# Kernel optimization log

Hardware: AMD Instinct MI355X
Metric: run time of the kernel (lower is better)

Reference implementation:

```python
import jax, jax.numpy as jnp
import numpy as np

NC = 2            # num_classes
CONF_THR = 0.7
IOU_THR = 0.2

_PI, _PJ = np.triu_indices(9, k=1)   # 36 candidate edge directions for min-area rect


def _decode_level(out, stride):
    # out: [C,h,w]; scale (x,y) channels by stride and add the pixel grid, flatten to [h*w, C]
    C, h, w = out.shape
    gw = (stride * jnp.arange(w, dtype=out.dtype))[None, :]
    gh = (stride * jnp.arange(h, dtype=out.dtype))[:, None]
    out = out.at[NC + 1].set(out[NC + 1] * stride + gw)
    out = out.at[NC + 2].set(out[NC + 2] * stride + gh)
    return out.reshape(C, -1).T


def _min_area_polygons(pts18):
    # pts18: (N,18) interleaved (a,b) coordinate pairs of 9 points.
    # Min-area enclosing rectangle: optimal rect is aligned with some point-pair direction;
    # brute-force all 36 pairs (superset of hull edges) -> exact result, fully vectorized.
    P = pts18.reshape(-1, 9, 2)                       # (N,9,2)
    d = P[:, _PJ] - P[:, _PI]                         # (N,36,2)
    nrm = jnp.sqrt(jnp.sum(d * d, -1) + 1e-12)
    c, s = d[..., 0] / nrm, d[..., 1] / nrm           # (N,36)
    a, b = P[..., 0][:, None, :], P[..., 1][:, None, :]   # (N,1,9)
    u = a * c[..., None] + b * s[..., None]           # rotate by -theta
    v = -a * s[..., None] + b * c[..., None]
    umin, umax = u.min(-1), u.max(-1)
    vmin, vmax = v.min(-1), v.max(-1)
    area = (umax - umin) * (vmax - vmin)              # (N,36)
    k = jnp.argmin(area, 1)[:, None]
    tk = lambda z: jnp.take_along_axis(z, k, 1)[:, 0]
    c, s, umin, umax, vmin, vmax = map(tk, (c, s, umin, umax, vmin, vmax))
    cu = jnp.stack([umin, umax, umax, umin], -1)      # rect corners in rotated frame
    cv = jnp.stack([vmin, vmin, vmax, vmax], -1)
    ca = cu * c[:, None] - cv * s[:, None]            # rotate back
    cb = cu * s[:, None] + cv * c[:, None]
    return jnp.stack([ca, cb], -1).reshape(-1, 8)     # (N,8) interleaved corners


def _points_in_quad(pts, quad):
    # pts (M,2), quad (4,2) convex with consistent winding -> (M,) bool
    e = jnp.roll(quad, -1, 0) - quad
    r = pts[:, None, :] - quad[None]
    cr = e[None, :, 0] * r[..., 1] - e[None, :, 1] * r[..., 0]
    return (cr >= 0).all(-1) | (cr <= 0).all(-1)


def _box_decoder(rect):
    # rect (N,8) -> (N,5) [cx, cy, w, h, angle]; y_first=True convention from the source
    w = jnp.sqrt((rect[:, 0] - rect[:, 2]) ** 2 + (rect[:, 1] - rect[:, 3]) ** 2)
    h = jnp.sqrt((rect[:, 4] - rect[:, 2]) ** 2 + (rect[:, 5] - rect[:, 3]) ** 2)
    cx = rect[:, 1:8:2].sum(1) * 0.25
    cy = rect[:, 0:8:2].sum(1) * 0.25
    ang = jnp.arctan((rect[:, 0] - rect[:, 2]) / (rect[:, 1] - rect[:, 3]))
    return jnp.stack([cx, cy, w, h, ang], -1)


def _rbox_corners(b):
    cx, cy, w, h, a = b[0], b[1], b[2], b[3], b[4]
    cs, sn = jnp.cos(a), jnp.sin(a)
    lx = jnp.array([-0.5, 0.5, 0.5, -0.5]) * w
    ly = jnp.array([-0.5, -0.5, 0.5, 0.5]) * h
    return jnp.stack([cx + lx * cs - ly * sn, cy + lx * sn + ly * cs], -1)  # (4,2)


def _quad_inter_area(A, B):
    # exact intersection area of two convex quads A,B (4,2):
    # candidates = corners of each inside the other + all 16 edge-edge intersections,
    # sorted by angle around their centroid, masked shoelace.
    inA = _points_in_quad(B, A)
    inB = _points_in_quad(A, B)
    rA = jnp.roll(A, -1, 0) - A
    rB = jnp.roll(B, -1, 0) - B
    qp = B[None] - A[:, None]                                  # (4,4,2)
    den = rA[:, None, 0] * rB[None, :, 1] - rA[:, None, 1] * rB[None, :, 0]
    dsafe = jnp.where(jnp.abs(den) < 1e-9, 1e-9, den)
    t = (qp[..., 0] * rB[None, :, 1] - qp[..., 1] * rB[None, :, 0]) / dsafe
    uu = (qp[..., 0] * rA[:, None, 1] - qp[..., 1] * rA[:, None, 0]) / dsafe
    okx = (jnp.abs(den) > 1e-9) & (t >= 0) & (t <= 1) & (uu >= 0) & (uu <= 1)
    X = A[:, None] + t[..., None] * rA[:, None]
    pts = jnp.concatenate([A, B, X.reshape(16, 2)], 0)          # (24,2)
    val = jnp.concatenate([inB, inA, okx.reshape(16)], 0)
    n = val.sum()
    cen = jnp.sum(jnp.where(val[:, None], pts, 0.0), 0) / jnp.maximum(n, 1)
    rel = pts - cen
    ang = jnp.where(val, jnp.arctan2(rel[:, 1], rel[:, 0]), 1e9)
    o = jnp.argsort(ang)
    rp, vs = rel[o], val[o]
    rp = jnp.where(vs[:, None], rp, rp[0])   # invalid slots -> first valid vertex (zero-area edges)
    nx = jnp.roll(rp, -1, 0)
    area = 0.5 * jnp.abs(jnp.sum(rp[:, 0] * nx[:, 1] - rp[:, 1] * nx[:, 0]))
    return jnp.where(n >= 3, area, 0.0)


def _forward(out3, out4, out5, off1_l3, off1_l4, off1_l5, offf_l3, offf_l4, offf_l5):
    outs = jnp.concatenate([_decode_level(out3[0], 4),
                            _decode_level(out4[0], 8),
                            _decode_level(out5[0], 16)], 0)          # (N, NC+3)
    flat = lambda z: z[0].reshape(18, -1).T
    off1 = jnp.concatenate([flat(off1_l3), flat(off1_l4), flat(off1_l5)], 0)
    offf = jnp.concatenate([flat(offf_l3), flat(offf_l4), flat(offf_l5)], 0) + off1
    N = outs.shape[0]
    x, y = outs[:, NC + 1], outs[:, NC + 2]
    offf = offf + jnp.tile(jnp.stack([y, x], -1), (1, 9))            # (y,x) interleaved, 9 points
    xs, ys = offf[:, 1:18:2], offf[:, 0:18:2]
    area = (xs.max(1) - xs.min(1)) * (ys.max(1) - ys.min(1)) / 40.0
    conf = outs[:, 0]
    conf_mask = conf > CONF_THR * jax.nn.sigmoid(area)
    rect = _min_area_polygons(offf)                                  # (N,8)
    boxes5 = _box_decoder(rect)                                      # (N,5)
    corners = jax.vmap(_rbox_corners)(boxes5)                        # (N,4,2)
    areas5 = boxes5[:, 2] * boxes5[:, 3]
    position = outs[:, NC + 1:]                                      # (N,2) = (x,y)
    pts_yx = jnp.stack([position[:, 1], position[:, 0]], -1)         # (y,x), matches rect plane
    quads = rect.reshape(N, 4, 2)
    order = jnp.argsort(jnp.where(conf_mask, conf, -jnp.inf))[::-1]

    def step(carry, i):
        suppressed, keep = carry
        active = jnp.logical_not(suppressed[i])
        keep = keep.at[i].set(active)
        inside = _points_in_quad(pts_yx, quads[i])                   # points_in_polygons
        inter = jax.vmap(lambda C: _quad_inter_area(corners[i], C))(corners)
        iou = inter / (areas5[i] + areas5 - inter + 1e-9)            # box_iou_rotated
        suppressed = suppressed | (active & (inside | (iou >= IOU_THR)))
        return (suppressed, keep), None

    init = (jnp.logical_not(conf_mask), jnp.zeros(N, dtype=bool))
    (_, keep), _ = jax.lax.scan(step, init, order)

    cls = outs[:, 1:NC + 1]
    maxc = cls.max(1)
    masks = jnp.stack([keep & (cls[:, i] == maxc) for i in range(NC)], 0)  # (NC,N)
    cnt = masks.sum(1)
    result = jnp.where(masks[:, :, None], position[None], 0.0)             # (NC,N,2) padded
    rect_out = rect * keep[:, None].astype(rect.dtype)                     # (N,8) padded
    return cnt, result, rect_out


def setup_inputs() -> dict:
    key = jax.random.key(0)
    shapes = [("out3", (1, NC + 3, 32, 32)), ("out4", (1, NC + 3, 16, 16)), ("out5", (1, NC + 3, 8, 8)),
              ("off1_l3", (1, 18, 32, 32)), ("off1_l4", (1, 18, 16, 16)), ("off1_l5", (1, 18, 8, 8)),
              ("offf_l3", (1, 18, 32, 32)), ("offf_l4", (1, 18, 16, 16)), ("offf_l5", (1, 18, 8, 8))]
    ks = jax.random.split(key, len(shapes))
    return {n: jax.random.normal(k, s, dtype=jnp.float32) for (n, s), k in zip(shapes, ks)}


def reference(out3, out4, out5, off1_l3, off1_l4, off1_l5, offf_l3, offf_l4, offf_l5):
    return _forward(out3, out4, out5, off1_l3, off1_l4, off1_l5, offf_l3, offf_l4, offf_l5)
```

## Files before the change

### kernel.cpp

```cpp
#include <hip/hip_runtime.h>
#include <math.h>

#define N_DET 1344
#define NW 21
#define MW_MAX 8
#define T2S 9
#define PAIR_CAP 40000


__device__ __forceinline__ bool pt_in_quad4(const float* qx, const float* qy,
                                            float px, float py) {
    bool allp = true, alln = true;
#pragma unroll
    for (int k = 0; k < 4; k++) {
        int k1 = (k + 1) & 3;
        float ex = qx[k1] - qx[k], ey = qy[k1] - qy[k];
        float rx = px - qx[k],     ry = py - qy[k];
        float cr = ex * ry - ey * rx;
        allp = allp && (cr >= 0.f);
        alln = alln && (cr <= 0.f);
    }
    return allp || alln;
}

__device__ float quad_inter_area(const float* Ax, const float* Ay,
                                 const float* Bx, const float* By) {
    float px[24], py[24];
    unsigned vmask = 0;
    int n = 0;
#pragma unroll
    for (int k = 0; k < 4; k++) {
        px[k] = Ax[k]; py[k] = Ay[k];
        if (pt_in_quad4(Bx, By, Ax[k], Ay[k])) { vmask |= 1u << k; n++; }
    }
#pragma unroll
    for (int k = 0; k < 4; k++) {
        px[4 + k] = Bx[k]; py[4 + k] = By[k];
        if (pt_in_quad4(Ax, Ay, Bx[k], By[k])) { vmask |= 1u << (4 + k); n++; }
    }
#pragma unroll
    for (int k = 0; k < 4; k++) {
        int k1 = (k + 1) & 3;
        float rax = Ax[k1] - Ax[k], ray = Ay[k1] - Ay[k];
#pragma unroll
        for (int l = 0; l < 4; l++) {
            int l1 = (l + 1) & 3;
            float rbx = Bx[l1] - Bx[l], rby = By[l1] - By[l];
            float qpx = Bx[l] - Ax[k],  qpy = By[l] - Ay[k];
            float den = rax * rby - ray * rbx;
            float ad  = fabsf(den);
            float dsafe = (ad < 1e-9f) ? 1e-9f : den;
            float t = (qpx * rby - qpy * rbx) / dsafe;
            float u = (qpx * ray - qpy * rax) / dsafe;
            bool ok = (ad > 1e-9f) && t >= 0.f && t <= 1.f && u >= 0.f && u <= 1.f;
            int id = 8 + k * 4 + l;
            px[id] = Ax[k] + t * rax;
            py[id] = Ay[k] + t * ray;
            if (ok) { vmask |= 1u << id; n++; }
        }
    }
    float cx = 0.f, cy = 0.f;
#pragma unroll
    for (int m = 0; m < 24; m++)
        if ((vmask >> m) & 1u) { cx += px[m]; cy += py[m]; }
    int mx = (n < 1) ? 1 : n;
    cx = cx / (float)mx;
    cy = cy / (float)mx;

    unsigned long long key[32];
    float sx[32], sy[32];
#pragma unroll
    for (int m = 0; m < 24; m++) {
        float rx = px[m] - cx, ry = py[m] - cy;
        float a = ((vmask >> m) & 1u) ? atan2f(ry, rx) : 1e9f;
        unsigned u = __float_as_uint(a);
        u = (u & 0x80000000u) ? ~u : (u | 0x80000000u);
        key[m] = (((unsigned long long)u) << 6) | (unsigned)m;
        sx[m] = rx; sy[m] = ry;
    }
#pragma unroll
    for (int m = 24; m < 32; m++) { key[m] = ~0ull; sx[m] = 0.f; sy[m] = 0.f; }

#pragma unroll
    for (int k = 2; k <= 32; k <<= 1) {
#pragma unroll
        for (int j = k >> 1; j > 0; j >>= 1) {
#pragma unroll
            for (int t = 0; t < 32; t++) {
                int l = t ^ j;
                if (l > t) {
                    bool up = ((t & k) == 0);
                    bool sw = up ? (key[t] > key[l]) : (key[t] < key[l]);
                    if (sw) {
                        unsigned long long tk = key[t]; key[t] = key[l]; key[l] = tk;
                        float tx = sx[t]; sx[t] = sx[l]; sx[l] = tx;
                        float ty = sy[t]; sy[t] = sy[l]; sy[l] = ty;
                    }
                }
            }
        }
    }

    unsigned ut = __float_as_uint(1e9f) | 0x80000000u;
    unsigned long long kt = ((unsigned long long)ut) << 6;
    float fx = sx[0], fy = sy[0];
    float qx2[24], qy2[24];
#pragma unroll
    for (int m = 0; m < 24; m++) {
        bool v = key[m] < kt;
        qx2[m] = v ? sx[m] : fx;
        qy2[m] = v ? sy[m] : fy;
    }
    float ssum = 0.f;
#pragma unroll
    for (int m = 0; m < 24; m++) {
        int m1 = (m + 1) % 24;
        ssum += qx2[m] * qy2[m1] - qy2[m] * qx2[m1];
    }
    float area = 0.5f * fabsf(ssum);
    return (n >= 3) ? area : 0.f;
}

__device__ bool iou_suppress(const float* __restrict__ cor, const float* __restrict__ a5,
                             int i, int j) {
    float Axr[4], Ayr[4], Bxr[4], Byr[4];
#pragma unroll
    for (int k = 0; k < 4; k++) {
        Axr[k] = cor[i * 8 + 2 * k]; Ayr[k] = cor[i * 8 + 2 * k + 1];
        Bxr[k] = cor[j * 8 + 2 * k]; Byr[k] = cor[j * 8 + 2 * k + 1];
    }
    float inter = quad_inter_area(Axr, Ayr, Bxr, Byr);
    float iou = inter / (a5[i] + a5[j] - inter + 1e-9f);
    return iou >= 0.2f;
}

__global__ void k_decode(const float* __restrict__ out3, const float* __restrict__ out4,
                         const float* __restrict__ out5,
                         const float* __restrict__ o1l3, const float* __restrict__ o1l4,
                         const float* __restrict__ o1l5,
                         const float* __restrict__ ofl3, const float* __restrict__ ofl4,
                         const float* __restrict__ ofl5,
                         float* conf, float* cls0, float* cls1, float* xx, float* yy,
                         float* a5, float* ccx, float* ccy, float* rr,
                         float* rect, float* cor, int* mask, int* Mcnt, int* pairCnt) {
    int n = blockIdx.x * blockDim.x + threadIdx.x;
    if (n >= N_DET) return;
    if (n == 0) { *Mcnt = 0; *pairCnt = 0; }
    const float *out, *o1, *of;
    int w, idx; float stride;
    if (n < 1024)      { out = out3; o1 = o1l3; of = ofl3; w = 32; idx = n;        stride = 4.f; }
    else if (n < 1280) { out = out4; o1 = o1l4; of = ofl4; w = 16; idx = n - 1024; stride = 8.f; }
    else               { out = out5; o1 = o1l5; of = ofl5; w = 8;  idx = n - 1280; stride = 16.f; }
    int hw = w * w;
    int row = idx / w, col = idx % w;
    float cf = out[0 * hw + idx];
    float c0 = out[1 * hw + idx];
    float c1 = out[2 * hw + idx];
    float x  = out[3 * hw + idx] * stride + stride * (float)col;
    float y  = out[4 * hw + idx] * stride + stride * (float)row;

    float Pa[9], Pb[9];
    float minb = INFINITY, maxb = -INFINITY, mina = INFINITY, maxa = -INFINITY;
#pragma unroll
    for (int k = 0; k < 9; k++) {
        float a = of[(2 * k) * hw + idx]     + o1[(2 * k) * hw + idx]     + y;
        float b = of[(2 * k + 1) * hw + idx] + o1[(2 * k + 1) * hw + idx] + x;
        Pa[k] = a; Pb[k] = b;
        mina = fminf(mina, a); maxa = fmaxf(maxa, a);
        minb = fminf(minb, b); maxb = fmaxf(maxb, b);
    }
    float area = (maxb - minb) * (maxa - mina) / 40.0f;
    float sg = 1.0f / (1.0f + expf(-area));
    int m = (cf > 0.7f * sg) ? 1 : 0;

    float best = INFINITY, bc = 0.f, bs = 0.f;
    float bumin = 0.f, bumax = 0.f, bvmin = 0.f, bvmax = 0.f;
#pragma unroll
    for (int i = 0; i < 9; i++) {
#pragma unroll
        for (int j = i + 1; j < 9; j++) {
            float d0 = Pa[j] - Pa[i], d1 = Pb[j] - Pb[i];
            float nr = sqrtf(d0 * d0 + d1 * d1 + 1e-12f);
            float c = d0 / nr, s = d1 / nr;
            float umin = INFINITY, umax = -INFINITY, vmin = INFINITY, vmax = -INFINITY;
#pragma unroll
            for (int k = 0; k < 9; k++) {
                float u =  Pa[k] * c + Pb[k] * s;
                float v = -Pa[k] * s + Pb[k] * c;
                umin = fminf(umin, u); umax = fmaxf(umax, u);
                vmin = fminf(vmin, v); vmax = fmaxf(vmax, v);
            }
            float ar = (umax - umin) * (vmax - vmin);
            if (ar < best) { best = ar; bc = c; bs = s;
                             bumin = umin; bumax = umax; bvmin = vmin; bvmax = vmax; }
        }
    }
    float cu[4] = {bumin, bumax, bumax, bumin};
    float cv[4] = {bvmin, bvmin, bvmax, bvmax};
    float r8[8];
#pragma unroll
    for (int k = 0; k < 4; k++) {
        r8[2 * k]     = cu[k] * bc - cv[k] * bs;
        r8[2 * k + 1] = cu[k] * bs + cv[k] * bc;
    }
    float w5 = sqrtf((r8[0] - r8[2]) * (r8[0] - r8[2]) + (r8[1] - r8[3]) * (r8[1] - r8[3]));
    float h5 = sqrtf((r8[4] - r8[2]) * (r8[4] - r8[2]) + (r8[5] - r8[3]) * (r8[5] - r8[3]));
    float cx = (r8[1] + r8[3] + r8[5] + r8[7]) * 0.25f;
    float cy = (r8[0] + r8[2] + r8[4] + r8[6]) * 0.25f;
    float ang = atanf((r8[0] - r8[2]) / (r8[1] - r8[3]));
    float cs = cosf(ang), sn = sinf(ang);
    const float lxs[4] = {-0.5f, 0.5f, 0.5f, -0.5f};
    const float lys[4] = {-0.5f, -0.5f, 0.5f, 0.5f};
#pragma unroll
    for (int k = 0; k < 4; k++) {
        cor[n * 8 + 2 * k]     = cx + lxs[k] * w5 * cs - lys[k] * h5 * sn;
        cor[n * 8 + 2 * k + 1] = cy + lxs[k] * w5 * sn + lys[k] * h5 * cs;
    }
#pragma unroll
    for (int k = 0; k < 8; k++) rect[n * 8 + k] = r8[k];
    conf[n] = cf; cls0[n] = c0; cls1[n] = c1;
    xx[n] = x; yy[n] = y; a5[n] = w5 * h5; mask[n] = m;
    ccx[n] = cx; ccy[n] = cy;
    rr[n] = 0.5f * sqrtf(w5 * w5 + h5 * h5);
}

__global__ __launch_bounds__(64) void k_order(const float* __restrict__ conf,
                                              const int* __restrict__ mask,
                                              int* order, int* Mcnt) {
    int b = blockIdx.x;
    int lane = threadIdx.x;
    int mb = mask[b];
    float ki = mb ? conf[b] : -INFINITY;
    int rank = 0;
    for (int j = lane; j < N_DET; j += 64) {
        float kj = mask[j] ? conf[j] : -INFINITY;
        rank += ((kj > ki) || (kj == ki && j > b)) ? 1 : 0;
    }
    for (int off = 32; off; off >>= 1) rank += __shfl_down(rank, off, 64);
    if (lane == 0) {
        order[rank] = b;
        if (mb) atomicAdd(Mcnt, 1);
    }
}

__global__ __launch_bounds__(256) void k_pairs_a(
        const float* __restrict__ rect, const float* __restrict__ cor,
        const float* __restrict__ a5,
        const float* __restrict__ xx, const float* __restrict__ yy,
        const float* __restrict__ ccx, const float* __restrict__ ccy,
        const float* __restrict__ rr,
        const int* __restrict__ order, const int* __restrict__ Mcnt,
        unsigned long long* __restrict__ S2, unsigned int* __restrict__ pairs,
        int* __restrict__ pairCnt) {
    int gw   = (blockIdx.x * 256 + threadIdx.x) >> 6;
    int lane = threadIdx.x & 63;
    int M = *Mcnt;
    int MW = (M + 63) >> 6;
    int p = gw / NW;
    int w = gw - p * NW;
    if (p >= M || w >= MW) return;
    bool use_list = (MW <= MW_MAX);
    int i = order[p];
    int q = w * 64 + lane;
    bool valid = q < M;
    int j = valid ? order[q] : i;

    float cxi = ccx[i], cyi = ccy[i], ri = rr[i];
    float dy0 = yy[j] - cyi, dx0 = xx[j] - cxi;
    float rin = ri + 0.1f;
    bool inside = false;
    if (dy0 * dy0 + dx0 * dx0 <= rin * rin) {
        float qxr[4], qyr[4];
#pragma unroll
        for (int k = 0; k < 4; k++) { qxr[k] = rect[i * 8 + 2 * k]; qyr[k] = rect[i * 8 + 2 * k + 1]; }
        inside = pt_in_quad4(qxr, qyr, yy[j], xx[j]);
    }
    bool bit = valid && inside;
    unsigned long long bb = __ballot(bit);
    if (lane == 0) S2[p * MW + w] = bb;

    float ex = cxi - ccx[j], ey = cyi - ccy[j];
    float rs = ri + rr[j] + 0.1f;
    bool iou_pos = valid && (q != p) && !bit && (ex * ex + ey * ey <= rs * rs);
    if (iou_pos) {
        if (use_list) {
            int pos = atomicAdd(pairCnt, 1);
            if (pos < PAIR_CAP) {
                pairs[pos] = ((unsigned)p << 11) | (unsigned)q;
            } else if (iou_suppress(cor, a5, i, j)) {
                atomicOr(&S2[p * MW + (q >> 6)], 1ull << (q & 63));
            }
        } else if (iou_suppress(cor, a5, i, j)) {
            atomicOr(&S2[p * MW + (q >> 6)], 1ull << (q & 63));
        }
    }
}

__global__ __launch_bounds__(256) void k_pairs_b(
        const float* __restrict__ cor, const float* __restrict__ a5,
        const int* __restrict__ order, const int* __restrict__ Mcnt,
        const int* __restrict__ pairCnt, const unsigned int* __restrict__ pairs,
        unsigned long long* __restrict__ S2) {
    int M = *Mcnt;
    int MW = (M + 63) >> 6;
    if (MW > MW_MAX) return;
    int cnt = *pairCnt; if (cnt > PAIR_CAP) cnt = PAIR_CAP;
    int stride = gridDim.x * 256;
    for (int t = blockIdx.x * 256 + threadIdx.x; t < cnt; t += stride) {
        unsigned v = pairs[t];
        int p = (int)(v >> 11), q = (int)(v & 2047u);
        int i = order[p], j = order[q];
        if (iou_suppress(cor, a5, i, j))
            atomicOr(&S2[p * MW + (q >> 6)], 1ull << (q & 63));
    }
}

__global__ __launch_bounds__(1024) void k_scan_out(
    const float* __restrict__ cls0, const float* __restrict__ cls1,
    const float* __restrict__ xx, const float* __restrict__ yy,
    const float* __restrict__ rect,
    const int* __restrict__ order, const int* __restrict__ Mcnt,
    const unsigned long long* __restrict__ S2, float* __restrict__ out) {
    __shared__ int order_s[N_DET];
    __shared__ unsigned long long T2[512 * T2S];
    __shared__ unsigned long long Kbuf[2][MW_MAX];
    __shared__ unsigned int keep32[(N_DET + 31) / 32];
    __shared__ int changed;
    __shared__ int cnt_s[2];
    int tid = threadIdx.x;
    int lane = tid & 63, wid = tid >> 6;
    int M = *Mcnt;
    int MW = (M + 63) >> 6;
    for (int t = tid; t < N_DET; t += 1024) order_s[t] = order[t];
    for (int t = tid; t < (N_DET + 31) / 32; t += 1024) keep32[t] = 0u;
    if (tid == 0) changed = 0;
    if (tid < 2) cnt_s[tid] = 0;
    __syncthreads();

    int cur = 0;
    if (M > 0 && MW <= MW_MAX) {
        for (int blk = wid; blk < MW * MW; blk += 16) {
            int wp = blk / MW, wq = blk - wp * MW;
            int pp = wp * 64 + lane;
            unsigned long long x = (pp < M) ? S2[pp * MW + wq] : 0ull;
#pragma unroll
            for (int b = 0; b < 64; b++) {
                unsigned long long bb = __ballot((x >> b) & 1ull);
                if (lane == b) T2[(wq * 64 + b) * T2S + wp] = bb;
            }
        }
        if (tid < MW_MAX) {
            int lo = tid * 64;
            unsigned long long iv = 0ull;
            if (M > lo) iv = (M - lo >= 64) ? ~0ull : ((1ull << (M - lo)) - 1ull);
            Kbuf[0][tid] = iv;
            Kbuf[1][tid] = 0ull;
        }
        __syncthreads();

        for (int it = 0; it <= M; ++it) {
            bool newk = false;
            if (tid < 512 && tid < M) {
                int q = tid, qw = q >> 6;
                unsigned long long sup = 0ull;
                for (int w = 0; w < qw; ++w) sup |= T2[q * T2S + w] & Kbuf[cur][w];
                unsigned long long pm = (q & 63) ? ((1ull << (q & 63)) - 1ull) : 0ull;
                sup |= T2[q * T2S + qw] & Kbuf[cur][qw] & pm;
                newk = (sup == 0ull);
            }
            unsigned long long bb = __ballot(newk);
            if (wid < MW_MAX && lane == 0) {
                if (bb != Kbuf[cur][wid]) changed = 1;
                Kbuf[cur ^ 1][wid] = bb;
            }
            __syncthreads();
            int ch = changed;
            __syncthreads();
            if (tid == 0) changed = 0;
            cur ^= 1;
            if (!ch) break;
            __syncthreads();
        }
        __syncthreads();
        if (tid < 512 && tid < M) {
            if ((Kbuf[cur][tid >> 6] >> (tid & 63)) & 1ull) {
                int i = order_s[tid];
                atomicOr(&keep32[i >> 5], 1u << (i & 31));
            }
        }
    } else if (M > 0) {
        if (tid < 64) {
            unsigned long long rem = 0ull;
            int lo = lane * 64;
            if (M > lo) rem = (M - lo >= 64) ? ~0ull : ((1ull << (M - lo)) - 1ull);
            for (int guard = 0; guard < N_DET; guard++) {
                unsigned long long vote = __ballot(rem != 0ull);
                if (!vote) break;
                int w = __builtin_ctzll(vote);
                unsigned long long wd = __shfl(rem, w, 64);
                int b = __builtin_ctzll(wd);
                int p = w * 64 + b;
                int i = order_s[p];
                if (lane == 0) atomicOr(&keep32[i >> 5], 1u << (i & 31));
                unsigned long long rowv = (lane < MW) ? S2[p * MW + lane] : 0ull;
                rem &= ~rowv;
                if (lane == w) rem &= ~(1ull << b);
            }
        }
    }
    __syncthreads();

    int c0 = 0, c1 = 0;
    for (int n = tid; n < N_DET; n += 1024) {
        bool kp = (keep32[n >> 5] >> (n & 31)) & 1u;
        float a = cls0[n], b = cls1[n];
        float mxc = fmaxf(a, b);
        bool m0 = kp && (a == mxc);
        bool m1 = kp && (b == mxc);
        float x = xx[n], y = yy[n];
        out[2 + 0 * N_DET * 2 + n * 2 + 0] = m0 ? x : 0.f;
        out[2 + 0 * N_DET * 2 + n * 2 + 1] = m0 ? y : 0.f;
        out[2 + 1 * N_DET * 2 + n * 2 + 0] = m1 ? x : 0.f;
        out[2 + 1 * N_DET * 2 + n * 2 + 1] = m1 ? y : 0.f;
        float kf = kp ? 1.f : 0.f;
#pragma unroll
        for (int k = 0; k < 8; k++)
            out[2 + 2 * N_DET * 2 + n * 8 + k] = rect[n * 8 + k] * kf;
        c0 += m0 ? 1 : 0;
        c1 += m1 ? 1 : 0;
    }
    if (c0) atomicAdd(&cnt_s[0], c0);
    if (c1) atomicAdd(&cnt_s[1], c1);
    __syncthreads();
    if (tid == 0) { out[0] = (float)cnt_s[0]; out[1] = (float)cnt_s[1]; }
}

extern "C" void kernel_launch(void* const* d_in, const int* in_sizes, int n_in,
                              void* d_out, int out_size, void* d_ws, size_t ws_size,
                              hipStream_t stream) {
    const float* out3 = (const float*)d_in[0];
    const float* out4 = (const float*)d_in[1];
    const float* out5 = (const float*)d_in[2];
    const float* o1l3 = (const float*)d_in[3];
    const float* o1l4 = (const float*)d_in[4];
    const float* o1l5 = (const float*)d_in[5];
    const float* ofl3 = (const float*)d_in[6];
    const float* ofl4 = (const float*)d_in[7];
    const float* ofl5 = (const float*)d_in[8];
    float* out = (float*)d_out;

    const int N = N_DET;
    float* wsf  = (float*)d_ws;
    float* conf = wsf + 0 * N;
    float* cls0 = wsf + 1 * N;
    float* cls1 = wsf + 2 * N;
    float* xx   = wsf + 3 * N;
    float* yy   = wsf + 4 * N;
    float* a5   = wsf + 5 * N;
    float* ccx  = wsf + 6 * N;
    float* ccy  = wsf + 7 * N;
    float* rr   = wsf + 8 * N;
    float* rect = wsf + 9 * N;
    float* cor  = wsf + 17 * N;
    int* mask   = (int*)(wsf + 25 * N);
    int* order  = mask + N;
    int* Mcnt   = order + N;
    int* pairCnt = Mcnt + 1;
    unsigned long long* S2 = (unsigned long long*)(wsf + 27 * N + 4);
    unsigned int* pairs = (unsigned int*)((char*)S2 + 32768);

    k_decode<<<(N + 255) / 256, 256, 0, stream>>>(out3, out4, out5, o1l3, o1l4, o1l5,
                                                  ofl3, ofl4, ofl5,
                                                  conf, cls0, cls1, xx, yy, a5,
                                                  ccx, ccy, rr, rect, cor, mask, Mcnt, pairCnt);
    k_order<<<N, 64, 0, stream>>>(conf, mask, order, Mcnt);
    k_pairs_a<<<(N * NW) / 4, 256, 0, stream>>>(rect, cor, a5, xx, yy, ccx, ccy, rr,
                                                order, Mcnt, S2, pairs, pairCnt);
    k_pairs_b<<<128, 256, 0, stream>>>(cor, a5, order, Mcnt, pairCnt, pairs, S2);
    k_scan_out<<<1, 1024, 0, stream>>>(cls0, cls1, xx, yy, rect, order, Mcnt, S2, out);
}
```

Before: 139.2 us.

## Use grid-stride pair kernel, wave-aggregated atomics, and single-wave fixed-point NMS scan

The pair kernel now runs on a fixed grid of 1024 blocks and strides over the live M*MW wave tasks, so it no longer launches blocks that return immediately. It also reserves pair-list slots with one atomic per wave instead of one per lane. The fixed-point keep iteration in the scan kernel now runs entirely inside one wavefront with the keep masks held in registers. This removes the three block-wide barriers per iteration, and the scan kernel shrinks to 512 threads. The trade-off is that the iterative resolve is serialized over up to eight 64-lane chunks within a single wave.

```diff
diff --git a/kernel.cpp b/kernel.cpp
--- a/kernel.cpp
+++ b/kernel.cpp
@@ -252,46 +252,58 @@
         const int* __restrict__ order, const int* __restrict__ Mcnt,
         unsigned long long* __restrict__ S2, unsigned int* __restrict__ pairs,
         int* __restrict__ pairCnt) {
-    int gw   = (blockIdx.x * 256 + threadIdx.x) >> 6;
-    int lane = threadIdx.x & 63;
     int M = *Mcnt;
+    if (M <= 0) return;
     int MW = (M + 63) >> 6;
-    int p = gw / NW;
-    int w = gw - p * NW;
-    if (p >= M || w >= MW) return;
     bool use_list = (MW <= MW_MAX);
-    int i = order[p];
-    int q = w * 64 + lane;
-    bool valid = q < M;
-    int j = valid ? order[q] : i;
-
-    float cxi = ccx[i], cyi = ccy[i], ri = rr[i];
-    float dy0 = yy[j] - cyi, dx0 = xx[j] - cxi;
-    float rin = ri + 0.1f;
-    bool inside = false;
-    if (dy0 * dy0 + dx0 * dx0 <= rin * rin) {
-        float qxr[4], qyr[4];
-#pragma unroll
-        for (int k = 0; k < 4; k++) { qxr[k] = rect[i * 8 + 2 * k]; qyr[k] = rect[i * 8 + 2 * k + 1]; }
-        inside = pt_in_quad4(qxr, qyr, yy[j], xx[j]);
-    }
-    bool bit = valid && inside;
-    unsigned long long bb = __ballot(bit);
-    if (lane == 0) S2[p * MW + w] = bb;
-
-    float ex = cxi - ccx[j], ey = cyi - ccy[j];
-    float rs = ri + rr[j] + 0.1f;
-    bool iou_pos = valid && (q != p) && !bit && (ex * ex + ey * ey <= rs * rs);
-    if (iou_pos) {
+    int lane  = threadIdx.x & 63;
+    int gwave = (blockIdx.x * 256 + threadIdx.x) >> 6;
+    int nwave = (gridDim.x * 256) >> 6;
+    int total = M * MW;
+    for (int t = gwave; t < total; t += nwave) {
+        int p = t / MW;
+        int w = t - p * MW;
+        int i = order[p];
+        int q = w * 64 + lane;
+        bool valid = q < M;
+        int j = valid ? order[q] : i;
+
+        float cbi = ccx[i], cai = ccy[i], ri = rr[i];
+        float da = yy[j] - cai, db = xx[j] - cbi;
+        float rin = ri + 0.1f;
+        bool inside = false;
+        if (da * da + db * db <= rin * rin) {
+            float qxr[4], qyr[4];
+#pragma unroll
+            for (int k = 0; k < 4; k++) { qxr[k] = rect[i * 8 + 2 * k]; qyr[k] = rect[i * 8 + 2 * k + 1]; }
+            inside = pt_in_quad4(qxr, qyr, yy[j], xx[j]);
+        }
+        bool bit = valid && inside;
+        unsigned long long bb = __ballot(bit);
+        if (lane == 0) S2[p * MW + w] = bb;
+
+        float ex = cbi - ccx[j], ey = cai - ccy[j];
+        float rs = ri + rr[j] + 0.1f;
+        bool iou_pos = valid && (q != p) && !bit && (ex * ex + ey * ey <= rs * rs);
         if (use_list) {
-            int pos = atomicAdd(pairCnt, 1);
-            if (pos < PAIR_CAP) {
-                pairs[pos] = ((unsigned)p << 11) | (unsigned)q;
-            } else if (iou_suppress(cor, a5, i, j)) {
-                atomicOr(&S2[p * MW + (q >> 6)], 1ull << (q & 63));
-            }
-        } else if (iou_suppress(cor, a5, i, j)) {
-            atomicOr(&S2[p * MW + (q >> 6)], 1ull << (q & 63));
+            unsigned long long pm = __ballot(iou_pos);
+            if (pm) {
+                int cw = __popcll(pm);
+                int base = 0;
+                if (lane == 0) base = atomicAdd(pairCnt, cw);
+                base = __shfl(base, 0, 64);
+                if (iou_pos) {
+                    int pos = base + __popcll(pm & ((1ull << lane) - 1ull));
+                    if (pos < PAIR_CAP) {
+                        pairs[pos] = ((unsigned)p << 11) | (unsigned)q;
+                    } else if (iou_suppress(cor, a5, i, j)) {
+                        atomicOr(&S2[p * MW + w], 1ull << (q & 63));
+                    }
+                }
+            }
+        } else if (iou_pos) {
+            if (iou_suppress(cor, a5, i, j))
+                atomicOr(&S2[p * MW + w], 1ull << (q & 63));
         }
     }
 }
@@ -315,7 +327,7 @@
     }
 }
 
-__global__ __launch_bounds__(1024) void k_scan_out(
+__global__ __launch_bounds__(512) void k_scan_out(
     const float* __restrict__ cls0, const float* __restrict__ cls1,
     const float* __restrict__ xx, const float* __restrict__ yy,
     const float* __restrict__ rect,
@@ -323,23 +335,21 @@
     const unsigned long long* __restrict__ S2, float* __restrict__ out) {
     __shared__ int order_s[N_DET];
     __shared__ unsigned long long T2[512 * T2S];
-    __shared__ unsigned long long Kbuf[2][MW_MAX];
+    __shared__ unsigned long long Kfin[MW_MAX];
     __shared__ unsigned int keep32[(N_DET + 31) / 32];
-    __shared__ int changed;
     __shared__ int cnt_s[2];
     int tid = threadIdx.x;
     int lane = tid & 63, wid = tid >> 6;
     int M = *Mcnt;
     int MW = (M + 63) >> 6;
-    for (int t = tid; t < N_DET; t += 1024) order_s[t] = order[t];
-    for (int t = tid; t < (N_DET + 31) / 32; t += 1024) keep32[t] = 0u;
-    if (tid == 0) changed = 0;
+    for (int t = tid; t < N_DET; t += 512) order_s[t] = order[t];
+    for (int t = tid; t < (N_DET + 31) / 32; t += 512) keep32[t] = 0u;
     if (tid < 2) cnt_s[tid] = 0;
+    if (tid < MW_MAX) Kfin[tid] = 0ull;
     __syncthreads();
 
-    int cur = 0;
     if (M > 0 && MW <= MW_MAX) {
-        for (int blk = wid; blk < MW * MW; blk += 16) {
+        for (int blk = wid; blk < MW * MW; blk += 8) {
             int wp = blk / MW, wq = blk - wp * MW;
             int pp = wp * 64 + lane;
             unsigned long long x = (pp < M) ? S2[pp * MW + wq] : 0ull;
@@ -349,47 +359,51 @@
                 if (lane == b) T2[(wq * 64 + b) * T2S + wp] = bb;
             }
         }
-        if (tid < MW_MAX) {
-            int lo = tid * 64;
-            unsigned long long iv = 0ull;
-            if (M > lo) iv = (M - lo >= 64) ? ~0ull : ((1ull << (M - lo)) - 1ull);
-            Kbuf[0][tid] = iv;
-            Kbuf[1][tid] = 0ull;
-        }
         __syncthreads();
 
-        for (int it = 0; it <= M; ++it) {
-            bool newk = false;
-            if (tid < 512 && tid < M) {
-                int q = tid, qw = q >> 6;
-                unsigned long long sup = 0ull;
-                for (int w = 0; w < qw; ++w) sup |= T2[q * T2S + w] & Kbuf[cur][w];
-                unsigned long long pm = (q & 63) ? ((1ull << (q & 63)) - 1ull) : 0ull;
-                sup |= T2[q * T2S + qw] & Kbuf[cur][qw] & pm;
-                newk = (sup == 0ull);
-            }
-            unsigned long long bb = __ballot(newk);
-            if (wid < MW_MAX && lane == 0) {
-                if (bb != Kbuf[cur][wid]) changed = 1;
-                Kbuf[cur ^ 1][wid] = bb;
-            }
-            __syncthreads();
-            int ch = changed;
-            __syncthreads();
-            if (tid == 0) changed = 0;
-            cur ^= 1;
-            if (!ch) break;
-            __syncthreads();
+        if (wid == 0) {
+            unsigned long long kw[MW_MAX];
+#pragma unroll
+            for (int w = 0; w < MW_MAX; w++) {
+                int lo = w * 64;
+                kw[w] = (M > lo) ? ((M - lo >= 64) ? ~0ull : ((1ull << (M - lo)) - 1ull)) : 0ull;
+            }
+            unsigned long long pmask = lane ? ((1ull << lane) - 1ull) : 0ull;
+            for (int it = 0; it <= M; ++it) {
+                bool changed = false;
+#pragma unroll
+                for (int k = 0; k < MW_MAX; k++) {
+                    if (k < MW) {
+                        int q = k * 64 + lane;
+                        const unsigned long long* row = &T2[q * T2S];
+                        unsigned long long sup = 0ull;
+#pragma unroll
+                        for (int w = 0; w < MW_MAX; w++) {
+                            if (w < k)       sup |= row[w] & kw[w];
+                            else if (w == k) sup |= row[w] & kw[w] & pmask;
+                        }
+                        bool nb = (q < M) && (sup == 0ull);
+                        unsigned long long nw = __ballot(nb);
+                        changed |= (nw != kw[k]);
+                        kw[k] = nw;
+                    }
+                }
+                if (!changed) break;
+            }
+            if (lane == 0) {
+#pragma unroll
+                for (int w = 0; w < MW_MAX; w++) Kfin[w] = kw[w];
+            }
         }
         __syncthreads();
-        if (tid < 512 && tid < M) {
-            if ((Kbuf[cur][tid >> 6] >> (tid & 63)) & 1ull) {
-                int i = order_s[tid];
+        for (int t = tid; t < M; t += 512) {
+            if ((Kfin[t >> 6] >> (t & 63)) & 1ull) {
+                int i = order_s[t];
                 atomicOr(&keep32[i >> 5], 1u << (i & 31));
             }
         }
     } else if (M > 0) {
-        if (tid < 64) {
+        if (wid == 0) {
             unsigned long long rem = 0ull;
             int lo = lane * 64;
             if (M > lo) rem = (M - lo >= 64) ? ~0ull : ((1ull << (M - lo)) - 1ull);
@@ -411,7 +425,7 @@
     __syncthreads();
 
     int c0 = 0, c1 = 0;
-    for (int n = tid; n < N_DET; n += 1024) {
+    for (int n = tid; n < N_DET; n += 512) {
         bool kp = (keep32[n >> 5] >> (n & 31)) & 1u;
         float a = cls0[n], b = cls1[n];
         float mxc = fmaxf(a, b);
@@ -474,8 +488,8 @@
                                                   conf, cls0, cls1, xx, yy, a5,
                                                   ccx, ccy, rr, rect, cor, mask, Mcnt, pairCnt);
     k_order<<<N, 64, 0, stream>>>(conf, mask, order, Mcnt);
-    k_pairs_a<<<(N * NW) / 4, 256, 0, stream>>>(rect, cor, a5, xx, yy, ccx, ccy, rr,
-                                                order, Mcnt, S2, pairs, pairCnt);
-    k_pairs_b<<<128, 256, 0, stream>>>(cor, a5, order, Mcnt, pairCnt, pairs, S2);
-    k_scan_out<<<1, 1024, 0, stream>>>(cls0, cls1, xx, yy, rect, order, Mcnt, S2, out);
-}
+    k_pairs_a<<<1024, 256, 0, stream>>>(rect, cor, a5, xx, yy, ccx, ccy, rr,
+                                        order, Mcnt, S2, pairs, pairCnt);
+    k_pairs_b<<<64, 256, 0, stream>>>(cor, a5, order, Mcnt, pairCnt, pairs, S2);
+    k_scan_out<<<1, 512, 0, stream>>>(cls0, cls1, xx, yy, rect, order, Mcnt, S2, out);
+}
```

Result: slower. 142.9 us (+2.7%).
